# Performance work log

Hardware: AMD Instinct MI355X
Metric: run time of the kernel (lower is better)

The kernel has to match this reference:

```python
import jax, jax.numpy as jnp
import numpy as np

N_NODES = 100000
N_EDGES = 3200000


def setup_inputs() -> dict:
    key = jax.random.key(0)
    k1, k2, k3, k4 = jax.random.split(key, 4)
    x = jax.random.normal(k1, (N_NODES, 16), dtype=jnp.float32)
    edge_index = jax.random.randint(k2, (2, N_EDGES), 0, N_NODES, dtype=jnp.int64)
    # Glorot-ish init like PyG's GCNConv linear layer
    W1 = jax.random.normal(k3, (16, 32), dtype=jnp.float32) * (1.0 / np.sqrt(16))
    b1 = jnp.zeros((32,), dtype=jnp.float32)
    W2 = jax.random.normal(k4, (32, 2), dtype=jnp.float32) * (1.0 / np.sqrt(32))
    b2 = jnp.zeros((2,), dtype=jnp.float32)
    return {"x": x, "edge_index": edge_index, "W1": W1, "b1": b1, "W2": W2, "b2": b2}


def _gcn_conv(x, W, b, src, dst, n):
    """PyG GCNConv: add self-loops, symmetric deg^{-1/2} normalization,
    linear transform, scatter-add aggregation, then bias."""
    h = x @ W  # [N, out]
    ones = jnp.ones(src.shape[0], dtype=x.dtype)
    deg = jax.ops.segment_sum(ones, dst, num_segments=n)  # in-degree incl. self-loops
    dinv = jnp.where(deg > 0, jax.lax.rsqrt(deg), 0.0)
    norm = dinv[src] * dinv[dst]  # [E+N]
    msg = h[src] * norm[:, None]  # gather + scale, [E+N, out]
    out = jax.ops.segment_sum(msg, dst, num_segments=n)  # scatter-add
    return out + b


def reference(x, edge_index, W1, b1, W2, b2):
    n = x.shape[0]
    loop = jnp.arange(n, dtype=edge_index.dtype)
    src = jnp.concatenate([edge_index[0], loop])  # self-loops appended
    dst = jnp.concatenate([edge_index[1], loop])
    h = jax.nn.relu(_gcn_conv(x, W1, b1, src, dst, n))
    return _gcn_conv(h, W2, b2, src, dst, n)
```

## Files before the change

kernel.cpp:

```cpp
#include <hip/hip_runtime.h>
#include <hip/hip_fp16.h>


#define B 256
#define NB_MAX 1024
#define BDIV 128
#define BSHIFT 7
#define CHUNK 4096
#define BCAP 6144
#define RI_MASK 0x7FFFFFu

__global__ __launch_bounds__(256) void k_phist(const int* __restrict__ dst,
                                               unsigned short* __restrict__ hists,
                                               int E, int NB, int NBLK) {
    __shared__ int h[NB_MAX];
    int tid = threadIdx.x, blk = blockIdx.x;
    for (int b = tid; b < NB; b += 256) h[b] = 0;
    __syncthreads();
    int start = blk * CHUNK;
    int end = min(start + CHUNK, E);
    for (int e = start + tid; e < end; e += 256)
        atomicAdd(&h[((unsigned)dst[e]) >> BSHIFT], 1);
    __syncthreads();
    for (int b = tid; b < NB; b += 256) hists[b * NBLK + blk] = (unsigned short)h[b];
}

__global__ __launch_bounds__(1024) void k_pscan1(unsigned short* __restrict__ hists,
                                                 int* __restrict__ totals, int NBLK) {
    __shared__ int s[1024];
    int b = blockIdx.x, tid = threadIdx.x;
    int v = (tid < NBLK) ? (int)hists[b * NBLK + tid] : 0;
    s[tid] = v;
    __syncthreads();
    for (int off = 1; off < 1024; off <<= 1) {
        int u = (tid >= off) ? s[tid - off] : 0;
        __syncthreads();
        s[tid] += u;
        __syncthreads();
    }
    if (tid < NBLK) hists[b * NBLK + tid] = (unsigned short)(s[tid] - v);
    if (tid == 1023) totals[b] = s[1023];
}

__global__ __launch_bounds__(1024) void k_pscan2(const int* __restrict__ totals,
                                                 int* __restrict__ base, int NB, int E) {
    __shared__ int s[1024];
    int tid = threadIdx.x;
    int v = (tid < NB) ? totals[tid] : 0;
    s[tid] = v;
    __syncthreads();
    for (int off = 1; off < 1024; off <<= 1) {
        int u = (tid >= off) ? s[tid - off] : 0;
        __syncthreads();
        s[tid] += u;
        __syncthreads();
    }
    if (tid < NB) base[tid] = s[tid] - v;
    if (tid == 1023) base[NB] = s[1023];
}

__global__ __launch_bounds__(256) void k_move(const int* __restrict__ src,
                                              const int* __restrict__ dst,
                                              const unsigned short* __restrict__ hists,
                                              const int* __restrict__ base,
                                              unsigned* __restrict__ packed,
                                              int E, int NB, int NBLK) {
    __shared__ unsigned stage[CHUNK];
    __shared__ unsigned short stage_b[CHUNK];
    __shared__ int lh[NB_MAX];
    __shared__ int lexc[NB_MAX];
    __shared__ int gb[NB_MAX];
    __shared__ int part[256];
    int tid = threadIdx.x, blk = blockIdx.x;
    int start = blk * CHUNK;
    int end = min(start + CHUNK, E);
    for (int b = tid; b < NB; b += 256) lh[b] = 0;
    __syncthreads();
    for (int e = start + tid; e < end; e += 256)
        atomicAdd(&lh[((unsigned)dst[e]) >> BSHIFT], 1);
    __syncthreads();
    int t4 = tid * 4;
    int a0 = 0, a1 = 0, a2 = 0, a3 = 0;
    if (t4 + 0 < NB) a0 = lh[t4 + 0];
    if (t4 + 1 < NB) a1 = lh[t4 + 1];
    if (t4 + 2 < NB) a2 = lh[t4 + 2];
    if (t4 + 3 < NB) a3 = lh[t4 + 3];
    int sum = a0 + a1 + a2 + a3;
    part[tid] = sum;
    __syncthreads();
    for (int off = 1; off < 256; off <<= 1) {
        int u = (tid >= off) ? part[tid - off] : 0;
        __syncthreads();
        part[tid] += u;
        __syncthreads();
    }
    int run = part[tid] - sum;
    if (t4 + 0 < NB) { lexc[t4 + 0] = run; run += a0; }
    if (t4 + 1 < NB) { lexc[t4 + 1] = run; run += a1; }
    if (t4 + 2 < NB) { lexc[t4 + 2] = run; run += a2; }
    if (t4 + 3 < NB) { lexc[t4 + 3] = run; run += a3; }
    __syncthreads();
    for (int b = tid; b < NB; b += 256) {
        lh[b] = lexc[b];
        gb[b] = base[b] + (int)hists[b * NBLK + blk] - lexc[b];
    }
    __syncthreads();
    for (int e = start + tid; e < end; e += 256) {
        unsigned d = (unsigned)dst[e];
        int b = d >> BSHIFT;
        int r = atomicAdd(&lh[b], 1);
        stage[r] = (unsigned)src[e] | ((d & (BDIV - 1u)) << 20);
        stage_b[r] = (unsigned short)b;
    }
    __syncthreads();
    int cnt = end - start;
    for (int i = tid; i < cnt; i += 256)
        packed[gb[stage_b[i]] + i] = stage[i];
}

__global__ __launch_bounds__(256) void k_bucket_csr(const unsigned* __restrict__ packed,
                                                    const int* __restrict__ base,
                                                    unsigned* __restrict__ rowinfo,
                                                    float* __restrict__ dinv,
                                                    int* __restrict__ col, int n) {
    __shared__ unsigned stg[BCAP];
    __shared__ int lcnt[BDIV];
    __shared__ int plexc[BDIV];
    int b = blockIdx.x, tid = threadIdx.x;
    if (tid < BDIV) lcnt[tid] = 0;
    __syncthreads();
    int s0 = base[b], s1 = base[b + 1];
    for (int i = s0 + tid; i < s1; i += 256) {
        unsigned u = packed[i];
        int k = i - s0;
        if (k < BCAP) stg[k] = u;
        atomicAdd(&lcnt[u >> 20], 1);
    }
    __syncthreads();
    int v = (tid < BDIV) ? lcnt[tid] : 0;
    int vp = (v + 7) & ~7;
    if (tid < BDIV) plexc[tid] = vp;
    __syncthreads();
    for (int off = 1; off < BDIV; off <<= 1) {
        int u = (tid < BDIV && tid >= off) ? plexc[tid - off] : 0;
        __syncthreads();
        if (tid < BDIV) plexc[tid] += u;
        __syncthreads();
    }
    int cb = s0 + 1024 * b;
    if (tid < BDIV) {
        plexc[tid] -= vp;
        int node = b * BDIV + tid;
        if (node < n) {
            rowinfo[node] = (unsigned)(cb + plexc[tid]) | ((unsigned)(vp >> 3) << 23);
            dinv[node] = rsqrtf((float)(v + 1));
        }
        lcnt[tid] = 0;
    }
    __syncthreads();
    for (int i = s0 + tid; i < s1; i += 256) {
        int k = i - s0;
        unsigned u = (k < BCAP) ? stg[k] : packed[i];
        int l = (int)(u >> 20);
        int pos = cb + plexc[l] + atomicAdd(&lcnt[l], 1);
        col[pos] = (int)(u & 0xFFFFFu);
    }
    __syncthreads();
    if (tid < BDIV) {
        int st = cb + plexc[tid];
        for (int k = v; k < vp; ++k) col[st + k] = n;
    }
}

__global__ void k_prep(const float* __restrict__ x, const float* __restrict__ dinv,
                       __half2* __restrict__ x16, float* __restrict__ t, int n8) {
    int g = blockIdx.x * blockDim.x + threadIdx.x;
    if (g < n8) {
        float d = dinv[g >> 3];
        float2 v = ((const float2*)x)[g];
        x16[g] = __float22half2_rn(make_float2(v.x * d, v.y * d));
    } else if (g < n8 + 8) {
        x16[g] = __float22half2_rn(make_float2(0.f, 0.f));
        if (g == n8) {
            t[(n8 >> 3) * 2 + 0] = 0.f;
            t[(n8 >> 3) * 2 + 1] = 0.f;
        }
    }
}

__global__ __launch_bounds__(256) void k_l1w(const __half2* __restrict__ x16,
                                             const unsigned* __restrict__ rowinfo,
                                             const int* __restrict__ col,
                                             const float* __restrict__ dinv,
                                             const float* __restrict__ W1,
                                             const float* __restrict__ b1,
                                             const float* __restrict__ W2,
                                             float* __restrict__ t, int n) {
    __shared__ float sW1[512], sW2[64], sb1[32];
    int tid = threadIdx.x;
    for (int k = tid; k < 512; k += 256) sW1[k] = W1[k];
    if (tid < 64) sW2[tid] = W2[tid];
    if (tid < 32) sb1[tid] = b1[tid];
    __syncthreads();
    int lane = tid & 63;
    int r = blockIdx.x * 4 + (tid >> 6);
    if (r >= n) return;
    int h = lane & 7, eg = lane >> 3;
    float dr = dinv[r];
    unsigned ri = rowinfo[r];
    int j = (int)(ri & RI_MASK) + eg;
    int trips = (int)(ri >> 23);
    float s0 = 0.f, s1 = 0.f;
    if (eg == 0) {
        float2 f = __half22float2(x16[(size_t)r * 8 + h]);
        s0 = f.x; s1 = f.y;
    }
#pragma unroll 4
    for (int it = 0; it < trips; ++it, j += 8) {
        int sc = col[j];
        float2 f = __half22float2(x16[(size_t)sc * 8 + h]);
        s0 += f.x; s1 += f.y;
    }
    s0 += __shfl_xor(s0, 8);  s1 += __shfl_xor(s1, 8);
    s0 += __shfl_xor(s0, 16); s1 += __shfl_xor(s1, 16);
    s0 += __shfl_xor(s0, 32); s1 += __shfl_xor(s1, 32);
    s0 *= dr; s1 *= dr;
    int j32 = lane & 31;
    float hv = sb1[j32];
#pragma unroll
    for (int k = 0; k < 16; ++k) {
        float a = __shfl((k & 1) ? s1 : s0, k >> 1);
        hv = fmaf(a, sW1[k * 32 + j32], hv);
    }
    hv = fmaxf(hv, 0.f);
    float p = hv * sW2[j32 * 2 + (lane >> 5)];
#pragma unroll
    for (int off = 1; off <= 16; off <<= 1) p += __shfl_xor(p, off);
    if ((lane & 31) == 0) t[(size_t)r * 2 + (lane >> 5)] = p * dr;
}

__global__ __launch_bounds__(256) void k_l2w(const unsigned* __restrict__ rowinfo,
                                             const int* __restrict__ col,
                                             const float* __restrict__ dinv,
                                             const float* __restrict__ ts,
                                             const float* __restrict__ b2,
                                             float* __restrict__ out, int n) {
    int g = blockIdx.x * 256 + threadIdx.x;
    int i = g >> 3, q = g & 7;
    if (i >= n) return;
    float di = dinv[i];
    unsigned ri = rowinfo[i];
    int j = (int)(ri & RI_MASK) + q;
    int trips = (int)(ri >> 23);
    float a0 = 0.f, a1 = 0.f;
    if (q == 0) {
        float2 tv = *(const float2*)(ts + (size_t)i * 2);
        a0 = tv.x; a1 = tv.y;
    }
#pragma unroll 4
    for (int it = 0; it < trips; ++it, j += 8) {
        int sc = col[j];
        float2 tv = *(const float2*)(ts + (size_t)sc * 2);
        a0 += tv.x; a1 += tv.y;
    }
    a0 += __shfl_xor(a0, 1); a1 += __shfl_xor(a1, 1);
    a0 += __shfl_xor(a0, 2); a1 += __shfl_xor(a1, 2);
    a0 += __shfl_xor(a0, 4); a1 += __shfl_xor(a1, 4);
    if (q == 0) {
        out[(size_t)i * 2 + 0] = fmaf(a0, di, b2[0]);
        out[(size_t)i * 2 + 1] = fmaf(a1, di, b2[1]);
    }
}


__global__ void k_zero(int* __restrict__ cnt, int n) {
    int i = blockIdx.x * blockDim.x + threadIdx.x;
    if (i < n) cnt[i] = 0;
}
__global__ void k_hist_rank(const int* __restrict__ dst, int* __restrict__ cnt,
                            int* __restrict__ rank, int E) {
    int e = blockIdx.x * blockDim.x + threadIdx.x;
    if (e < E) rank[e] = atomicAdd(&cnt[dst[e]], 1);
}
__global__ __launch_bounds__(256) void k_blocksum(const int* __restrict__ cnt,
                                                  int* __restrict__ bsum, int n) {
    __shared__ int s[256];
    int tid = threadIdx.x;
    int bse = blockIdx.x * 1024 + tid * 4;
    int sum = 0;
#pragma unroll
    for (int q = 0; q < 4; ++q) {
        int i = bse + q;
        if (i < n) sum += (cnt[i] + 7) & ~7;
    }
    s[tid] = sum;
    __syncthreads();
    for (int off = 128; off > 0; off >>= 1) {
        if (tid < off) s[tid] += s[tid + off];
        __syncthreads();
    }
    if (tid == 0) bsum[blockIdx.x] = s[0];
}
__global__ __launch_bounds__(1024) void k_scan_bsums(const int* __restrict__ bsum,
                                                     int* __restrict__ boff, int nb) {
    __shared__ int s[1024];
    int tid = threadIdx.x;
    int v = (tid < nb) ? bsum[tid] : 0;
    s[tid] = v;
    __syncthreads();
    for (int off = 1; off < 1024; off <<= 1) {
        int u = (tid >= off) ? s[tid - off] : 0;
        __syncthreads();
        s[tid] += u;
        __syncthreads();
    }
    if (tid < nb) boff[tid] = s[tid] - v;
}
__global__ __launch_bounds__(256) void k_scan_apply(const int* __restrict__ cnt,
                                                    const int* __restrict__ boff,
                                                    unsigned* __restrict__ rowinfo,
                                                    float* __restrict__ dinv, int n) {
    __shared__ int s[256];
    int tid = threadIdx.x;
    int bse = blockIdx.x * 1024 + tid * 4;
    int c[4];
    int sum = 0;
#pragma unroll
    for (int q = 0; q < 4; ++q) {
        int i = bse + q;
        c[q] = (i < n) ? ((cnt[i] + 7) & ~7) : 0;
        sum += c[q];
    }
    s[tid] = sum;
    __syncthreads();
    for (int off = 1; off < 256; off <<= 1) {
        int u = (tid >= off) ? s[tid - off] : 0;
        __syncthreads();
        s[tid] += u;
        __syncthreads();
    }
    int run = boff[blockIdx.x] + s[tid] - sum;
#pragma unroll
    for (int q = 0; q < 4; ++q) {
        int i = bse + q;
        if (i < n) {
            rowinfo[i] = (unsigned)run | ((unsigned)(c[q] >> 3) << 23);
            run += c[q];
            dinv[i] = rsqrtf((float)(cnt[i] + 1));
        }
    }
}
__global__ void k_fill_rank(const int* __restrict__ src, const int* __restrict__ dst,
                            const unsigned* __restrict__ rowinfo,
                            const int* __restrict__ rank,
                            int* __restrict__ col, int E) {
    int e = blockIdx.x * blockDim.x + threadIdx.x;
    if (e >= E) return;
    int d = dst[e];
    col[(rowinfo[d] & RI_MASK) + rank[e]] = src[e];
}
__global__ void k_pad_sent(const unsigned* __restrict__ rowinfo,
                           const int* __restrict__ cnt,
                           int* __restrict__ col, int n) {
    int i = blockIdx.x * blockDim.x + threadIdx.x;
    if (i >= n) return;
    int st = (int)(rowinfo[i] & RI_MASK);
    int v = cnt[i], vp = (v + 7) & ~7;
    for (int k = v; k < vp; ++k) col[st + k] = n;
}

static inline size_t align4(size_t v) { return (v + 3) & ~(size_t)3; }

extern "C" void kernel_launch(void* const* d_in, const int* in_sizes, int n_in,
                              void* d_out, int out_size, void* d_ws, size_t ws_size,
                              hipStream_t stream) {
    const float* x  = (const float*)d_in[0];
    const int*   ei = (const int*)d_in[1];
    const float* W1 = (const float*)d_in[2];
    const float* b1 = (const float*)d_in[3];
    const float* W2 = (const float*)d_in[4];
    const float* b2 = (const float*)d_in[5];
    float* out = (float*)d_out;

    const int n = in_sizes[0] / 16;
    const int E = in_sizes[1] / 2;
    const int* src = ei;
    const int* dst = ei + E;

    const int gn = (n + B - 1) / B;
    const int ge = (E + B - 1) / B;
    const int n8 = n * 8;

    const int NB   = (n + BDIV - 1) / BDIV;
    const int NBLK = (E + CHUNK - 1) / CHUNK;

    size_t o_hists  = 0;
    size_t o_totals = align4(o_hists + ((size_t)NB * NBLK + 1) / 2);
    size_t o_base   = align4(o_totals + NB);
    size_t o_rowinf = align4(o_base + NB + 1);
    size_t o_dinv   = align4(o_rowinf + n);
    size_t o_packed = align4(o_dinv + n);
    size_t o_col    = align4(o_packed + E);
    size_t colsz    = (size_t)E + 1024 * (size_t)NB;
    size_t need_r5  = (o_col + colsz) * 4 + 64;
    size_t reuse_need = align4(2 * (size_t)n + 2) + (8 * (size_t)n + 8);

    bool r5_ok = (NB <= NB_MAX) && (NBLK <= 1024) && (n <= (1 << 20)) &&
                 ((size_t)E + 1024 * (size_t)NB < (RI_MASK + 1)) &&
                 (reuse_need <= (size_t)E) && (ws_size >= need_r5);

    if (r5_ok) {
        int* ws = (int*)d_ws;
        unsigned short* hists = (unsigned short*)(ws + o_hists);
        int*      totals = ws + o_totals;
        int*      base   = ws + o_base;
        unsigned* rowinf = (unsigned*)(ws + o_rowinf);
        float*    dinv   = (float*)(ws + o_dinv);
        unsigned* packed = (unsigned*)(ws + o_packed);
        int*      col    = ws + o_col;
        float*    t      = (float*)packed;
        __half2*  x16    = (__half2*)(packed + align4(2 * (size_t)n + 2));

        k_phist<<<NBLK, 256, 0, stream>>>(dst, hists, E, NB, NBLK);
        k_pscan1<<<NB, 1024, 0, stream>>>(hists, totals, NBLK);
        k_pscan2<<<1, 1024, 0, stream>>>(totals, base, NB, E);
        k_move<<<NBLK, 256, 0, stream>>>(src, dst, hists, base, packed, E, NB, NBLK);
        k_bucket_csr<<<NB, 256, 0, stream>>>(packed, base, rowinf, dinv, col, n);
        k_prep<<<(n8 + 8 + 255) / 256, 256, 0, stream>>>(x, dinv, x16, t, n8);
        k_l1w<<<(n + 3) / 4, 256, 0, stream>>>(x16, rowinf, col, dinv, W1, b1, W2, t, n);
        k_l2w<<<(8 * n + 255) / 256, 256, 0, stream>>>(rowinf, col, dinv, t, b2, out, n);
        return;
    }

    const int nb = (n + 1023) / 1024;
    size_t f_cnt    = 0;
    size_t f_rowinf = align4(f_cnt + n);
    size_t f_col    = align4(f_rowinf + n);
    size_t f_dinv   = align4(f_col + E + 8 * (size_t)n);
    size_t f_bsum   = align4(f_dinv + n);
    size_t f_boff   = align4(f_bsum + nb);
    size_t f_rank   = align4(f_boff + nb);
    size_t reuse2   = align4(2 * (size_t)n + 2) + (8 * (size_t)n + 8);
    size_t rmax = (size_t)E > reuse2 ? (size_t)E : reuse2;
    size_t need_rank = (f_rank + rmax) * 4 + 64;
    if (ws_size >= need_rank && nb <= 1024) {
        int*      ws     = (int*)d_ws;
        int*      cnt    = ws + f_cnt;
        unsigned* rowinf = (unsigned*)(ws + f_rowinf);
        int*      col    = ws + f_col;
        float*    dinv   = (float*)(ws + f_dinv);
        int*      bsum   = ws + f_bsum;
        int*      boff   = ws + f_boff;
        int*      rank   = ws + f_rank;
        float*    t      = (float*)rank;
        __half2*  x16    = (__half2*)(rank + align4(2 * (size_t)n + 2));

        k_zero<<<gn, B, 0, stream>>>(cnt, n);
        k_hist_rank<<<ge, B, 0, stream>>>(dst, cnt, rank, E);
        k_blocksum<<<nb, 256, 0, stream>>>(cnt, bsum, n);
        k_scan_bsums<<<1, 1024, 0, stream>>>(bsum, boff, nb);
        k_scan_apply<<<nb, 256, 0, stream>>>(cnt, boff, rowinf, dinv, n);
        k_fill_rank<<<ge, B, 0, stream>>>(src, dst, rowinf, rank, col, E);
        k_pad_sent<<<gn, B, 0, stream>>>(rowinf, cnt, col, n);
        k_prep<<<(n8 + 8 + 255) / 256, 256, 0, stream>>>(x, dinv, x16, t, n8);
        k_l1w<<<(n + 3) / 4, 256, 0, stream>>>(x16, rowinf, col, dinv, W1, b1, W2, t, n);
        k_l2w<<<(8 * n + 255) / 256, 256, 0, stream>>>(rowinf, col, dinv, t, b2, out, n);
    }
}
```

Before: 145.5 us.

## Fold bucket base scan into consumers and split layer-1 MLP into own kernel

Removes the single-block k_pscan2 launch by having k_move and k_bucket_csr each recompute the prefix sum over bucket totals redundantly in shared memory. Also splits the layer-1 dense MLP out of the gather kernel k_l1w into a new per-node k_mlp kernel, with the aggregated 16-wide features written to a scratch buffer. The first change saves one serial launch at the cost of a redundant scan per block. The second adds an extra launch and a round trip of n*16 floats through global memory, in exchange for a lighter gather kernel with no weight loads or shuffle-heavy matmul.

```diff
diff --git a/kernel.cpp b/kernel.cpp
--- a/kernel.cpp
+++ b/kernel.cpp
@@ -42,27 +42,10 @@
     if (tid == 1023) totals[b] = s[1023];
 }
 
-__global__ __launch_bounds__(1024) void k_pscan2(const int* __restrict__ totals,
-                                                 int* __restrict__ base, int NB, int E) {
-    __shared__ int s[1024];
-    int tid = threadIdx.x;
-    int v = (tid < NB) ? totals[tid] : 0;
-    s[tid] = v;
-    __syncthreads();
-    for (int off = 1; off < 1024; off <<= 1) {
-        int u = (tid >= off) ? s[tid - off] : 0;
-        __syncthreads();
-        s[tid] += u;
-        __syncthreads();
-    }
-    if (tid < NB) base[tid] = s[tid] - v;
-    if (tid == 1023) base[NB] = s[1023];
-}
-
 __global__ __launch_bounds__(256) void k_move(const int* __restrict__ src,
                                               const int* __restrict__ dst,
                                               const unsigned short* __restrict__ hists,
-                                              const int* __restrict__ base,
+                                              const int* __restrict__ totals,
                                               unsigned* __restrict__ packed,
                                               int E, int NB, int NBLK) {
     __shared__ unsigned stage[CHUNK];
@@ -72,37 +55,59 @@
     __shared__ int gb[NB_MAX];
     __shared__ int part[256];
     int tid = threadIdx.x, blk = blockIdx.x;
+    int t4 = tid * 4;
+    {
+        int a0 = (t4 + 0 < NB) ? totals[t4 + 0] : 0;
+        int a1 = (t4 + 1 < NB) ? totals[t4 + 1] : 0;
+        int a2 = (t4 + 2 < NB) ? totals[t4 + 2] : 0;
+        int a3 = (t4 + 3 < NB) ? totals[t4 + 3] : 0;
+        int sum = a0 + a1 + a2 + a3;
+        part[tid] = sum;
+        __syncthreads();
+        for (int off = 1; off < 256; off <<= 1) {
+            int u = (tid >= off) ? part[tid - off] : 0;
+            __syncthreads();
+            part[tid] += u;
+            __syncthreads();
+        }
+        int run = part[tid] - sum;
+        if (t4 + 0 < NB) { gb[t4 + 0] = run; run += a0; }
+        if (t4 + 1 < NB) { gb[t4 + 1] = run; run += a1; }
+        if (t4 + 2 < NB) { gb[t4 + 2] = run; run += a2; }
+        if (t4 + 3 < NB) { gb[t4 + 3] = run; run += a3; }
+    }
+    for (int b = tid; b < NB; b += 256) lh[b] = 0;
+    __syncthreads();
     int start = blk * CHUNK;
     int end = min(start + CHUNK, E);
-    for (int b = tid; b < NB; b += 256) lh[b] = 0;
-    __syncthreads();
     for (int e = start + tid; e < end; e += 256)
         atomicAdd(&lh[((unsigned)dst[e]) >> BSHIFT], 1);
     __syncthreads();
-    int t4 = tid * 4;
-    int a0 = 0, a1 = 0, a2 = 0, a3 = 0;
-    if (t4 + 0 < NB) a0 = lh[t4 + 0];
-    if (t4 + 1 < NB) a1 = lh[t4 + 1];
-    if (t4 + 2 < NB) a2 = lh[t4 + 2];
-    if (t4 + 3 < NB) a3 = lh[t4 + 3];
-    int sum = a0 + a1 + a2 + a3;
-    part[tid] = sum;
-    __syncthreads();
-    for (int off = 1; off < 256; off <<= 1) {
-        int u = (tid >= off) ? part[tid - off] : 0;
-        __syncthreads();
-        part[tid] += u;
-        __syncthreads();
-    }
-    int run = part[tid] - sum;
-    if (t4 + 0 < NB) { lexc[t4 + 0] = run; run += a0; }
-    if (t4 + 1 < NB) { lexc[t4 + 1] = run; run += a1; }
-    if (t4 + 2 < NB) { lexc[t4 + 2] = run; run += a2; }
-    if (t4 + 3 < NB) { lexc[t4 + 3] = run; run += a3; }
+    {
+        int a0 = 0, a1 = 0, a2 = 0, a3 = 0;
+        if (t4 + 0 < NB) a0 = lh[t4 + 0];
+        if (t4 + 1 < NB) a1 = lh[t4 + 1];
+        if (t4 + 2 < NB) a2 = lh[t4 + 2];
+        if (t4 + 3 < NB) a3 = lh[t4 + 3];
+        int sum = a0 + a1 + a2 + a3;
+        part[tid] = sum;
+        __syncthreads();
+        for (int off = 1; off < 256; off <<= 1) {
+            int u = (tid >= off) ? part[tid - off] : 0;
+            __syncthreads();
+            part[tid] += u;
+            __syncthreads();
+        }
+        int run = part[tid] - sum;
+        if (t4 + 0 < NB) { lexc[t4 + 0] = run; run += a0; }
+        if (t4 + 1 < NB) { lexc[t4 + 1] = run; run += a1; }
+        if (t4 + 2 < NB) { lexc[t4 + 2] = run; run += a2; }
+        if (t4 + 3 < NB) { lexc[t4 + 3] = run; run += a3; }
+    }
     __syncthreads();
     for (int b = tid; b < NB; b += 256) {
+        gb[b] = gb[b] + (int)hists[b * NBLK + blk] - lexc[b];
         lh[b] = lexc[b];
-        gb[b] = base[b] + (int)hists[b * NBLK + blk] - lexc[b];
     }
     __syncthreads();
     for (int e = start + tid; e < end; e += 256) {
@@ -119,17 +124,42 @@
 }
 
 __global__ __launch_bounds__(256) void k_bucket_csr(const unsigned* __restrict__ packed,
-                                                    const int* __restrict__ base,
+                                                    const int* __restrict__ totals,
                                                     unsigned* __restrict__ rowinfo,
                                                     float* __restrict__ dinv,
-                                                    int* __restrict__ col, int n) {
+                                                    int* __restrict__ col, int n, int NB) {
     __shared__ unsigned stg[BCAP];
+    __shared__ int part[256];
     __shared__ int lcnt[BDIV];
     __shared__ int plexc[BDIV];
+    __shared__ int sbase[2];
     int b = blockIdx.x, tid = threadIdx.x;
+    int t4 = tid * 4;
+    {
+        int a0 = (t4 + 0 < NB) ? totals[t4 + 0] : 0;
+        int a1 = (t4 + 1 < NB) ? totals[t4 + 1] : 0;
+        int a2 = (t4 + 2 < NB) ? totals[t4 + 2] : 0;
+        int a3 = (t4 + 3 < NB) ? totals[t4 + 3] : 0;
+        int sum = a0 + a1 + a2 + a3;
+        part[tid] = sum;
+        __syncthreads();
+        for (int off = 1; off < 256; off <<= 1) {
+            int u = (tid >= off) ? part[tid - off] : 0;
+            __syncthreads();
+            part[tid] += u;
+            __syncthreads();
+        }
+        int run = part[tid] - sum;
+        int a[4] = {a0, a1, a2, a3};
+#pragma unroll
+        for (int q = 0; q < 4; ++q) {
+            if (t4 + q == b) { sbase[0] = run; sbase[1] = run + a[q]; }
+            run += a[q];
+        }
+    }
     if (tid < BDIV) lcnt[tid] = 0;
     __syncthreads();
-    int s0 = base[b], s1 = base[b + 1];
+    int s0 = sbase[0], s1 = sbase[1];
     for (int i = s0 + tid; i < s1; i += 256) {
         unsigned u = packed[i];
         int k = i - s0;
@@ -192,16 +222,8 @@
                                              const unsigned* __restrict__ rowinfo,
                                              const int* __restrict__ col,
                                              const float* __restrict__ dinv,
-                                             const float* __restrict__ W1,
-                                             const float* __restrict__ b1,
-                                             const float* __restrict__ W2,
-                                             float* __restrict__ t, int n) {
-    __shared__ float sW1[512], sW2[64], sb1[32];
+                                             float* __restrict__ agg, int n) {
     int tid = threadIdx.x;
-    for (int k = tid; k < 512; k += 256) sW1[k] = W1[k];
-    if (tid < 64) sW2[tid] = W2[tid];
-    if (tid < 32) sb1[tid] = b1[tid];
-    __syncthreads();
     int lane = tid & 63;
     int r = blockIdx.x * 4 + (tid >> 6);
     if (r >= n) return;
@@ -224,19 +246,45 @@
     s0 += __shfl_xor(s0, 8);  s1 += __shfl_xor(s1, 8);
     s0 += __shfl_xor(s0, 16); s1 += __shfl_xor(s1, 16);
     s0 += __shfl_xor(s0, 32); s1 += __shfl_xor(s1, 32);
-    s0 *= dr; s1 *= dr;
-    int j32 = lane & 31;
-    float hv = sb1[j32];
-#pragma unroll
-    for (int k = 0; k < 16; ++k) {
-        float a = __shfl((k & 1) ? s1 : s0, k >> 1);
-        hv = fmaf(a, sW1[k * 32 + j32], hv);
-    }
-    hv = fmaxf(hv, 0.f);
-    float p = hv * sW2[j32 * 2 + (lane >> 5)];
-#pragma unroll
-    for (int off = 1; off <= 16; off <<= 1) p += __shfl_xor(p, off);
-    if ((lane & 31) == 0) t[(size_t)r * 2 + (lane >> 5)] = p * dr;
+    if (eg == 0)
+        *(float2*)(agg + (size_t)r * 16 + 2 * h) = make_float2(s0 * dr, s1 * dr);
+}
+
+__global__ __launch_bounds__(256) void k_mlp(const float* __restrict__ agg,
+                                             const float* __restrict__ dinv,
+                                             const float* __restrict__ W1,
+                                             const float* __restrict__ b1,
+                                             const float* __restrict__ W2,
+                                             float* __restrict__ t, int n) {
+    __shared__ float sW1[512], sW2[64], sb1[32];
+    int tid = threadIdx.x;
+    for (int k = tid; k < 512; k += 256) sW1[k] = W1[k];
+    if (tid < 64) sW2[tid] = W2[tid];
+    if (tid < 32) sb1[tid] = b1[tid];
+    __syncthreads();
+    int i = blockIdx.x * 256 + tid;
+    if (i >= n) return;
+    float a[16];
+    const float4* av = (const float4*)(agg + (size_t)i * 16);
+#pragma unroll
+    for (int q = 0; q < 4; ++q) {
+        float4 v = av[q];
+        a[4 * q + 0] = v.x; a[4 * q + 1] = v.y;
+        a[4 * q + 2] = v.z; a[4 * q + 3] = v.w;
+    }
+    float di = dinv[i];
+    float t0 = 0.f, t1 = 0.f;
+#pragma unroll
+    for (int j = 0; j < 32; ++j) {
+        float acc = sb1[j];
+#pragma unroll
+        for (int k = 0; k < 16; ++k) acc = fmaf(a[k], sW1[k * 32 + j], acc);
+        float hh = fmaxf(acc, 0.f);
+        t0 = fmaf(hh, sW2[j * 2 + 0], t0);
+        t1 = fmaf(hh, sW2[j * 2 + 1], t1);
+    }
+    t[(size_t)i * 2 + 0] = t0 * di;
+    t[(size_t)i * 2 + 1] = t1 * di;
 }
 
 __global__ __launch_bounds__(256) void k_l2w(const unsigned* __restrict__ rowinfo,
@@ -396,14 +444,16 @@
 
     size_t o_hists  = 0;
     size_t o_totals = align4(o_hists + ((size_t)NB * NBLK + 1) / 2);
-    size_t o_base   = align4(o_totals + NB);
-    size_t o_rowinf = align4(o_base + NB + 1);
+    size_t o_rowinf = align4(o_totals + NB);
     size_t o_dinv   = align4(o_rowinf + n);
     size_t o_packed = align4(o_dinv + n);
     size_t o_col    = align4(o_packed + E);
     size_t colsz    = (size_t)E + 1024 * (size_t)NB;
     size_t need_r5  = (o_col + colsz) * 4 + 64;
-    size_t reuse_need = align4(2 * (size_t)n + 2) + (8 * (size_t)n + 8);
+    size_t u_t   = 0;
+    size_t u_x16 = align4(2 * (size_t)n + 2);
+    size_t u_agg = align4(u_x16 + 8 * (size_t)n + 8);
+    size_t reuse_need = u_agg + 16 * (size_t)n;
 
     bool r5_ok = (NB <= NB_MAX) && (NBLK <= 1024) && (n <= (1 << 20)) &&
                  ((size_t)E + 1024 * (size_t)NB < (RI_MASK + 1)) &&
@@ -413,21 +463,21 @@
         int* ws = (int*)d_ws;
         unsigned short* hists = (unsigned short*)(ws + o_hists);
         int*      totals = ws + o_totals;
-        int*      base   = ws + o_base;
         unsigned* rowinf = (unsigned*)(ws + o_rowinf);
         float*    dinv   = (float*)(ws + o_dinv);
         unsigned* packed = (unsigned*)(ws + o_packed);
         int*      col    = ws + o_col;
-        float*    t      = (float*)packed;
-        __half2*  x16    = (__half2*)(packed + align4(2 * (size_t)n + 2));
+        float*    t      = (float*)(packed + u_t);
+        __half2*  x16    = (__half2*)(packed + u_x16);
+        float*    agg    = (float*)(packed + u_agg);
 
         k_phist<<<NBLK, 256, 0, stream>>>(dst, hists, E, NB, NBLK);
         k_pscan1<<<NB, 1024, 0, stream>>>(hists, totals, NBLK);
-        k_pscan2<<<1, 1024, 0, stream>>>(totals, base, NB, E);
-        k_move<<<NBLK, 256, 0, stream>>>(src, dst, hists, base, packed, E, NB, NBLK);
-        k_bucket_csr<<<NB, 256, 0, stream>>>(packed, base, rowinf, dinv, col, n);
+        k_move<<<NBLK, 256, 0, stream>>>(src, dst, hists, totals, packed, E, NB, NBLK);
+        k_bucket_csr<<<NB, 256, 0, stream>>>(packed, totals, rowinf, dinv, col, n, NB);
         k_prep<<<(n8 + 8 + 255) / 256, 256, 0, stream>>>(x, dinv, x16, t, n8);
-        k_l1w<<<(n + 3) / 4, 256, 0, stream>>>(x16, rowinf, col, dinv, W1, b1, W2, t, n);
+        k_l1w<<<(n + 3) / 4, 256, 0, stream>>>(x16, rowinf, col, dinv, agg, n);
+        k_mlp<<<gn, 256, 0, stream>>>(agg, dinv, W1, b1, W2, t, n);
         k_l2w<<<(8 * n + 255) / 256, 256, 0, stream>>>(rowinf, col, dinv, t, b2, out, n);
         return;
     }
@@ -440,7 +490,7 @@
     size_t f_bsum   = align4(f_dinv + n);
     size_t f_boff   = align4(f_bsum + nb);
     size_t f_rank   = align4(f_boff + nb);
-    size_t reuse2   = align4(2 * (size_t)n + 2) + (8 * (size_t)n + 8);
+    size_t reuse2   = align4(2 * (size_t)n + 2) + align4(8 * (size_t)n + 8) + 16 * (size_t)n;
     size_t rmax = (size_t)E > reuse2 ? (size_t)E : reuse2;
     size_t need_rank = (f_rank + rmax) * 4 + 64;
     if (ws_size >= need_rank && nb <= 1024) {
@@ -454,6 +504,7 @@
         int*      rank   = ws + f_rank;
         float*    t      = (float*)rank;
         __half2*  x16    = (__half2*)(rank + align4(2 * (size_t)n + 2));
+        float*    agg    = (float*)(rank + align4(2 * (size_t)n + 2) + align4(8 * (size_t)n + 8));
 
         k_zero<<<gn, B, 0, stream>>>(cnt, n);
         k_hist_rank<<<ge, B, 0, stream>>>(dst, cnt, rank, E);
@@ -463,7 +514,8 @@
         k_fill_rank<<<ge, B, 0, stream>>>(src, dst, rowinf, rank, col, E);
         k_pad_sent<<<gn, B, 0, stream>>>(rowinf, cnt, col, n);
         k_prep<<<(n8 + 8 + 255) / 256, 256, 0, stream>>>(x, dinv, x16, t, n8);
-        k_l1w<<<(n + 3) / 4, 256, 0, stream>>>(x16, rowinf, col, dinv, W1, b1, W2, t, n);
+        k_l1w<<<(n + 3) / 4, 256, 0, stream>>>(x16, rowinf, col, dinv, agg, n);
+        k_mlp<<<gn, 256, 0, stream>>>(agg, dinv, W1, b1, W2, t, n);
         k_l2w<<<(8 * n + 255) / 256, 256, 0, stream>>>(rowinf, col, dinv, t, b2, out, n);
     }
 }
```

New measurement: 132.5 us. -8.9%, faster.
